# Kernel tuning notes

Hardware: AMD Instinct MI355X
Metric: run time of the kernel (lower is better)

## Reference

```python
import jax, jax.numpy as jnp
import numpy as np

EPS = 0.5
MIN_SAMPLES = 5


def setup_inputs() -> dict:
    key = jax.random.key(0)
    X = jax.random.uniform(key, (12288, 8), dtype=jnp.float32)
    return {"X": X}


def reference(X):
    """DBSCAN: eps-range queries + cluster expansion, expressed as
    eps-graph connected components over core points (same clustering
    as the serial BFS in the original module; cluster ids are assigned
    in order of each cluster's minimum core index, matching the
    ascending-scan discovery order of the original)."""
    N = X.shape[0]
    SENTINEL = jnp.int32(N)

    # pairwise squared Euclidean distances [N, N] (KDTree range query equivalent)
    sq = jnp.sum(X * X, axis=1)
    d2 = sq[:, None] + sq[None, :] - 2.0 * (X @ X.T)
    adj = d2 <= (EPS * EPS)                      # eps-neighborhood (includes self)

    density = jnp.sum(adj, axis=1)               # |query_ball_point(x_i, eps)|
    core = density >= MIN_SAMPLES                # core-point mask

    # core-core edges: BFS expansion only propagates through cores
    core_adj = adj & core[None, :] & core[:, None]

    idx = jnp.arange(N, dtype=jnp.int32)
    init = jnp.where(core, idx, SENTINEL)        # each core starts as its own root

    def prop(lbl):
        # min label over core neighbors (min-plus propagation = connected components)
        nb_min = jnp.min(jnp.where(core_adj, lbl[None, :], SENTINEL), axis=1)
        return jnp.minimum(lbl, nb_min)

    def cond(state):
        cur, prev = state
        return jnp.any(cur != prev)

    def body(state):
        cur, _ = state
        return prop(cur), cur

    lbl, _ = jax.lax.while_loop(cond, body, (prop(init), init))

    # border points: non-core points within eps of a core join that core's cluster
    core_nb = jnp.min(jnp.where(adj & core[None, :], lbl[None, :], SENTINEL), axis=1)
    root = jnp.where(core, lbl, core_nb)         # SENTINEL -> noise

    # compact cluster ids: rank of each cluster root (min core index) ascending,
    # matching the original's sequential discovery order k = 0, 1, ...
    is_root = core & (lbl == idx)
    rank = jnp.cumsum(is_root.astype(jnp.int32)) - 1   # rank[i] valid where is_root[i]
    labels = jnp.where(root < SENTINEL,
                       rank[jnp.clip(root, 0, N - 1)],
                       jnp.int32(-1))
    return labels
```

## Files before the change

kernel.cpp:

```cpp
#include <hip/hip_runtime.h>

#define NPTS 12288
#define DIMS 8
#define EPS2 0.25f
#define MINS 5
#define NIB1 (NPTS / 256)
#define NW   (NPTS / 32)
#define SENT NPTS
#define RMAX 512
#define W    (RMAX / 32)
#define BIGL 0x3fffffff
#define FT   128
#define FB   256
#define FBGRID 256

#define ATHR 128
#define AROWS 4
#define ATI  (ATHR * AROWS)
#define ANIB (NPTS / ATI)
#define ANJB 48
#define AJC  (NPTS / ANJB)
#define AWCH (AJC / 32)

__device__ __forceinline__ float dist2(const float* xi, const float4& a, const float4& b,
                                       float sqi, float sqj) {
  float dot = 0.f;
  dot = fmaf(xi[0], a.x, dot); dot = fmaf(xi[1], a.y, dot);
  dot = fmaf(xi[2], a.z, dot); dot = fmaf(xi[3], a.w, dot);
  dot = fmaf(xi[4], b.x, dot); dot = fmaf(xi[5], b.y, dot);
  dot = fmaf(xi[6], b.z, dot); dot = fmaf(xi[7], b.w, dot);
  return (sqi + sqj) - 2.0f * dot;
}


__global__ __launch_bounds__(ATHR) void k_adj(const float* __restrict__ X,
                                              unsigned int* __restrict__ adj,
                                              int* __restrict__ density) {
  __shared__ float4 xs[AJC][2];
  __shared__ float sqs[AJC];
  int t = threadIdx.x;
  int j0 = blockIdx.y * AJC;
  for (int s = t; s < AJC; s += ATHR) {
    int j = j0 + s;
    float4 a = ((const float4*)X)[j * 2];
    float4 b = ((const float4*)X)[j * 2 + 1];
    xs[s][0] = a; xs[s][1] = b;
    float sv = 0.f;
    sv = fmaf(a.x, a.x, sv); sv = fmaf(a.y, a.y, sv); sv = fmaf(a.z, a.z, sv); sv = fmaf(a.w, a.w, sv);
    sv = fmaf(b.x, b.x, sv); sv = fmaf(b.y, b.y, sv); sv = fmaf(b.z, b.z, sv); sv = fmaf(b.w, b.w, sv);
    sqs[s] = sv;
  }
  int ib = blockIdx.x * ATI + t;
  float xi[AROWS][DIMS];
  float sqi[AROWS];
#pragma unroll
  for (int r = 0; r < AROWS; r++) {
    int i = ib + r * ATHR;
#pragma unroll
    for (int d = 0; d < DIMS; d++) xi[r][d] = X[i * DIMS + d];
    float sv = 0.f;
#pragma unroll
    for (int d = 0; d < DIMS; d++) sv = fmaf(xi[r][d], xi[r][d], sv);
    sqi[r] = sv;
  }
  __syncthreads();
  unsigned int acc[AROWS][AWCH];
#pragma unroll
  for (int w = 0; w < AWCH; w++) {
    unsigned int b0 = 0u, b1 = 0u, b2 = 0u, b3 = 0u;
#pragma unroll 4
    for (int bit = 0; bit < 32; bit++) {
      int jj = (w << 5) + bit;
      float4 xa = xs[jj][0], xb = xs[jj][1];
      float sj = sqs[jj];
      unsigned int m = 1u << bit;
      if (dist2(xi[0], xa, xb, sqi[0], sj) <= EPS2) b0 |= m;
      if (dist2(xi[1], xa, xb, sqi[1], sj) <= EPS2) b1 |= m;
      if (dist2(xi[2], xa, xb, sqi[2], sj) <= EPS2) b2 |= m;
      if (dist2(xi[3], xa, xb, sqi[3], sj) <= EPS2) b3 |= m;
    }
    acc[0][w] = b0; acc[1][w] = b1; acc[2][w] = b2; acc[3][w] = b3;
  }
#pragma unroll
  for (int r = 0; r < AROWS; r++) {
    int i = ib + r * ATHR;
    uint4* dst = (uint4*)(adj + (size_t)i * NW + blockIdx.y * AWCH);
    dst[0] = make_uint4(acc[r][0], acc[r][1], acc[r][2], acc[r][3]);
    dst[1] = make_uint4(acc[r][4], acc[r][5], acc[r][6], acc[r][7]);
    int pc = 0;
#pragma unroll
    for (int w = 0; w < AWCH; w++) pc += __popc(acc[r][w]);
    atomicAdd(&density[i], pc);
  }
}

__global__ __launch_bounds__(256) void k_core(const int* __restrict__ density,
                                              unsigned long long* __restrict__ corebm,
                                              unsigned int* __restrict__ bm) {
  int t = threadIdx.x;
  if (blockIdx.x == 0) {
#pragma unroll
    for (int q = 0; q < RMAX * W / 256; q++) bm[t + q * 256] = 0u;
  }
  int i = blockIdx.x * 256 + t;
  unsigned long long m = __ballot(density[i] >= MINS);
  if ((t & 63) == 0) corebm[i >> 6] = m;
}

__global__ __launch_bounds__(256) void k_hookbm(const unsigned int* __restrict__ adj,
                                                const unsigned int* __restrict__ cb32,
                                                int* __restrict__ hook) {
  __shared__ unsigned int cb[NW];
  int t = threadIdx.x;
  for (int w = t; w < NW; w += 256) cb[w] = cb32[w];
  __syncthreads();
  int i = blockIdx.x * 256 + t;
  const unsigned int* row = adj + (size_t)i * NW;
  int m = i;
  for (int w = 0; w < NW; w++) {
    unsigned int x = row[w] & cb[w];
    if (x) { m = min(m, (w << 5) + __ffs(x) - 1); break; }
  }
  hook[i] = m;
}

__global__ __launch_bounds__(256) void k_compress(const int* __restrict__ density,
                                                  const int* __restrict__ hook,
                                                  int* __restrict__ L0) {
  int i = blockIdx.x * blockDim.x + threadIdx.x;
  if (i >= NPTS) return;
  if (density[i] >= MINS) {
    int v = i;
    int h = hook[v];
    while (h != v) { v = h; h = hook[v]; }
    L0[i] = v;
  } else {
    L0[i] = i;
  }
}

__global__ __launch_bounds__(1024) void k_rid(const int* __restrict__ density,
                                              const int* __restrict__ L0,
                                              int* __restrict__ Rptr,
                                              int* __restrict__ labL,
                                              int* __restrict__ bcount) {
  __shared__ unsigned short ridS[NPTS];
  __shared__ int wsum[16];
  int t = threadIdx.x;
  int lane = t & 63, wid = t >> 6;
  const int SEG = NPTS / 1024;
  int base = t * SEG;
  int flags = 0;
  int s = 0;
#pragma unroll
  for (int k = 0; k < SEG; k++) {
    int i = base + k;
    int f = (density[i] >= MINS && L0[i] == i) ? 1 : 0;
    flags |= f << k;
    s += f;
  }
  int segsum = s;
#pragma unroll
  for (int off = 1; off < 64; off <<= 1) {
    int n = __shfl_up(s, off, 64);
    if (lane >= off) s += n;
  }
  if (lane == 63) wsum[wid] = s;
  __syncthreads();
  int woff = 0;
  for (int w = 0; w < wid; w++) woff += wsum[w];
  int run = woff + s - segsum;
#pragma unroll
  for (int k = 0; k < SEG; k++) {
    ridS[base + k] = (unsigned short)run;
    run += (flags >> k) & 1;
  }
  if (t == 1023) *Rptr = run;
  if (t == 0) *bcount = 0;
  __syncthreads();
#pragma unroll
  for (int k = 0; k < SEG; k++) {
    int i = base + k;
    labL[i] = (density[i] >= MINS) ? min((int)ridS[L0[i]], RMAX - 1) : -1;
  }
}

__global__ __launch_bounds__(FB) void k_fillbm(const unsigned int* __restrict__ adj,
                                               const unsigned int* __restrict__ cb32,
                                               const int* __restrict__ labL,
                                               unsigned int* __restrict__ bm) {
  __shared__ unsigned int bmL[RMAX * W];
  __shared__ unsigned short labS[NPTS];
  __shared__ unsigned int cb[NW];
  int t = threadIdx.x;
  for (int q = t; q < RMAX * W; q += FB) bmL[q] = 0u;
  for (int q = t; q < NPTS; q += FB) labS[q] = (unsigned short)(labL[q] + 1);
  for (int w = t; w < NW; w += FB) cb[w] = cb32[w];
  __syncthreads();
  int lane = t & 63, wv = t >> 6;
  int gw = blockIdx.x * 4 + wv;
  for (int i = gw; i < NPTS; i += 4 * FBGRID) {
    int a0 = (int)labS[i] - 1;
    if (a0 < 0) continue;
    const unsigned int* row = adj + (size_t)i * NW;
    int wi = i >> 5;
    for (int w = wi + lane; w < NW; w += 64) {
      unsigned int x = row[w] & cb[w];
      if (w == wi) x &= (0xFFFFFFFEu << (i & 31));
      while (x) {
        int b = __ffs(x) - 1; x &= x - 1;
        int lj = (int)labS[(w << 5) + b] - 1;
        if (lj != a0) {
          atomicOr(&bmL[a0 * W + (lj >> 5)], 1u << (lj & 31));
          atomicOr(&bmL[lj * W + (a0 >> 5)], 1u << (a0 & 31));
        }
      }
    }
  }
  __syncthreads();
  for (int q = t; q < RMAX * W; q += FB) {
    unsigned int v = bmL[q];
    if (v) atomicOr(&bm[q], v);
  }
}

__global__ __launch_bounds__(RMAX) void k_cc(const unsigned int* __restrict__ bm,
                                             const int* __restrict__ Rptr,
                                             int* __restrict__ clab) {
  __shared__ int lbl[RMAX];
  __shared__ int mn[RMAX];
  __shared__ int chg, cmp;
  int a = threadIdx.x;
  int R = *Rptr; if (R > RMAX) R = RMAX;
  lbl[a] = a;
  __syncthreads();
  while (true) {
    int m = lbl[a];
    if (a < R) {
      const unsigned int* row = bm + a * W;
#pragma unroll
      for (int w = 0; w < W; w++) {
        unsigned int bits = row[w];
        while (bits) {
          int b = __ffs(bits) - 1;
          bits &= bits - 1;
          m = min(m, lbl[(w << 5) + b]);
        }
      }
    }
    mn[a] = m;
    if (a == 0) chg = 0;
    __syncthreads();
    int l = lbl[a];
    if (m < l) { atomicMin(&lbl[l], m); atomicMin(&lbl[a], m); chg = 1; }
    __syncthreads();
    while (true) {
      if (a == 0) cmp = 0;
      __syncthreads();
      int nl = lbl[lbl[a]];
      __syncthreads();
      if (nl < lbl[a]) { lbl[a] = nl; cmp = 1; }
      __syncthreads();
      if (!cmp) break;
    }
    if (!chg) break;
    __syncthreads();
  }
  int flag = (a < R && lbl[a] == a) ? 1 : 0;
  mn[a] = flag;
  __syncthreads();
  for (int off = 1; off < RMAX; off <<= 1) {
    int v = mn[a];
    int add = (a >= off) ? mn[a - off] : 0;
    __syncthreads();
    mn[a] = v + add;
    __syncthreads();
  }
  clab[a] = mn[lbl[a]] - 1;
}

__global__ __launch_bounds__(256) void k_labels(const int* __restrict__ labL,
                                                const int* __restrict__ clab,
                                                int* __restrict__ labArr,
                                                int* __restrict__ blist,
                                                int* __restrict__ bcount,
                                                float* __restrict__ out) {
  int i = blockIdx.x * blockDim.x + threadIdx.x;
  if (i >= NPTS) return;
  int a = labL[i];
  if (a >= 0) {
    int lab = clab[a];
    labArr[i] = lab;
    out[i] = (float)lab;
  } else {
    labArr[i] = BIGL;
    out[i] = -1.0f;
    int pos = atomicAdd(bcount, 1);
    blist[pos] = i;
  }
}

__global__ __launch_bounds__(FT) void k_border(const unsigned int* __restrict__ adj,
                                               const unsigned int* __restrict__ cb32,
                                               const int* __restrict__ labArr,
                                               const int* __restrict__ blist,
                                               const int* __restrict__ bcount,
                                               float* __restrict__ out) {
  __shared__ unsigned int cb[NW];
  __shared__ int wm[FT / 64];
  int t = threadIdx.x;
  for (int w = t; w < NW; w += FT) cb[w] = cb32[w];
  __syncthreads();
  int count = *bcount;
  for (int k = blockIdx.x; k < count; k += gridDim.x) {
    int p = blist[k];
    const unsigned int* row = adj + (size_t)p * NW;
    int m = BIGL;
    for (int w = t; w < NW; w += FT) {
      unsigned int x = row[w] & cb[w];
      while (x) {
        int b = __ffs(x) - 1; x &= x - 1;
        m = min(m, labArr[(w << 5) + b]);
      }
    }
#pragma unroll
    for (int off = 32; off >= 1; off >>= 1) m = min(m, __shfl_xor(m, off, 64));
    if ((t & 63) == 0) wm[t >> 6] = m;
    __syncthreads();
    if (t == 0) {
      int mm = min(wm[0], wm[1]);
      out[p] = (mm < BIGL) ? (float)mm : -1.0f;
    }
    __syncthreads();
  }
}


extern "C" void kernel_launch(void* const* d_in, const int* in_sizes, int n_in,
                              void* d_out, int out_size, void* d_ws, size_t ws_size,
                              hipStream_t stream) {
  const float* X = (const float*)d_in[0];
  float* out = (float*)d_out;

  char* ws = (char*)d_ws;
  unsigned int* adj = (unsigned int*)ws;
  size_t off = (size_t)NPTS * NW * 4;
  int* density = (int*)(ws + off);           off += 4 * NPTS;
  int* hook    = (int*)(ws + off);           off += 4 * NPTS;
  int* L0      = (int*)(ws + off);           off += 4 * NPTS;
  int* labL    = (int*)(ws + off);           off += 4 * NPTS;
  int* blist   = (int*)(ws + off);           off += 4 * NPTS;
  unsigned long long* corebm = (unsigned long long*)(ws + off); off += 2048;
  unsigned int* bm  = (unsigned int*)(ws + off); off += 4 * RMAX * W;
  int* clab    = (int*)(ws + off);           off += 4 * RMAX;
  int* Rptr    = (int*)(ws + off);
  int* bcount  = Rptr + 1;
  int* labArr  = L0;

  hipMemsetAsync(density, 0, 4 * NPTS, stream);

  dim3 gridA(ANIB, ANJB);

  k_adj<<<gridA, ATHR, 0, stream>>>(X, adj, density);
  k_core<<<NIB1, 256, 0, stream>>>(density, corebm, bm);
  k_hookbm<<<NIB1, 256, 0, stream>>>(adj, (const unsigned int*)corebm, hook);
  k_compress<<<NIB1, 256, 0, stream>>>(density, hook, L0);
  k_rid<<<1, 1024, 0, stream>>>(density, L0, Rptr, labL, bcount);
  k_fillbm<<<FBGRID, FB, 0, stream>>>(adj, (const unsigned int*)corebm, labL, bm);
  k_cc<<<1, RMAX, 0, stream>>>(bm, Rptr, clab);
  k_labels<<<NIB1, 256, 0, stream>>>(labL, clab, labArr, blist, bcount, out);
  k_border<<<256, FT, 0, stream>>>(adj, (const unsigned int*)corebm, labArr, blist, bcount, out);
}
```

Measured before the change: 240.3 us.

## Use packed FMA in adjacency kernel, bound hook scan, fuse compress into rid

The adjacency kernel now uses 256 threads with 2 rows each and computes dot products with two-wide float vector FMAs, which can map to packed fp32 instructions. The hook kernel scans only the words up to the point's own index, since only lower-index core neighbours can lower the hook. The separate pointer-chasing compress kernel is removed and its root-finding loop moved into the single-block rid kernel, saving one launch but running serial chains inside one block. labArr gets its own buffer now that L0 is gone.

```diff
diff --git a/kernel.cpp b/kernel.cpp
--- a/kernel.cpp
+++ b/kernel.cpp
@@ -14,22 +14,23 @@
 #define FB   256
 #define FBGRID 256
 
-#define ATHR 128
-#define AROWS 4
+#define ATHR 256
+#define AROWS 2
 #define ATI  (ATHR * AROWS)
 #define ANIB (NPTS / ATI)
 #define ANJB 48
 #define AJC  (NPTS / ANJB)
 #define AWCH (AJC / 32)
 
-__device__ __forceinline__ float dist2(const float* xi, const float4& a, const float4& b,
-                                       float sqi, float sqj) {
-  float dot = 0.f;
-  dot = fmaf(xi[0], a.x, dot); dot = fmaf(xi[1], a.y, dot);
-  dot = fmaf(xi[2], a.z, dot); dot = fmaf(xi[3], a.w, dot);
-  dot = fmaf(xi[4], b.x, dot); dot = fmaf(xi[5], b.y, dot);
-  dot = fmaf(xi[6], b.z, dot); dot = fmaf(xi[7], b.w, dot);
-  return (sqi + sqj) - 2.0f * dot;
+typedef float v2f __attribute__((ext_vector_type(2)));
+
+__device__ __forceinline__ float dot8(const v2f* xi, const float4& a, const float4& b) {
+  v2f y0 = {a.x, a.y}, y1 = {a.z, a.w}, y2 = {b.x, b.y}, y3 = {b.z, b.w};
+  v2f d = xi[0] * y0;
+  d = __builtin_elementwise_fma(xi[1], y1, d);
+  d = __builtin_elementwise_fma(xi[2], y2, d);
+  d = __builtin_elementwise_fma(xi[3], y3, d);
+  return d.x + d.y;
 }
 
 
@@ -40,58 +41,61 @@
   __shared__ float sqs[AJC];
   int t = threadIdx.x;
   int j0 = blockIdx.y * AJC;
-  for (int s = t; s < AJC; s += ATHR) {
-    int j = j0 + s;
+  {
+    int j = j0 + t;
     float4 a = ((const float4*)X)[j * 2];
     float4 b = ((const float4*)X)[j * 2 + 1];
-    xs[s][0] = a; xs[s][1] = b;
+    xs[t][0] = a; xs[t][1] = b;
     float sv = 0.f;
     sv = fmaf(a.x, a.x, sv); sv = fmaf(a.y, a.y, sv); sv = fmaf(a.z, a.z, sv); sv = fmaf(a.w, a.w, sv);
     sv = fmaf(b.x, b.x, sv); sv = fmaf(b.y, b.y, sv); sv = fmaf(b.z, b.z, sv); sv = fmaf(b.w, b.w, sv);
-    sqs[s] = sv;
-  }
-  int ib = blockIdx.x * ATI + t;
-  float xi[AROWS][DIMS];
-  float sqi[AROWS];
-#pragma unroll
-  for (int r = 0; r < AROWS; r++) {
-    int i = ib + r * ATHR;
-#pragma unroll
-    for (int d = 0; d < DIMS; d++) xi[r][d] = X[i * DIMS + d];
-    float sv = 0.f;
-#pragma unroll
-    for (int d = 0; d < DIMS; d++) sv = fmaf(xi[r][d], xi[r][d], sv);
-    sqi[r] = sv;
-  }
-  __syncthreads();
-  unsigned int acc[AROWS][AWCH];
+    sqs[t] = sv;
+  }
+  int i0 = blockIdx.x * ATI + t, i1 = i0 + ATHR;
+  v2f xi0[4], xi1[4];
+  {
+    float4 a0 = ((const float4*)X)[i0 * 2], b0v = ((const float4*)X)[i0 * 2 + 1];
+    float4 a1 = ((const float4*)X)[i1 * 2], b1v = ((const float4*)X)[i1 * 2 + 1];
+    xi0[0] = (v2f){a0.x, a0.y}; xi0[1] = (v2f){a0.z, a0.w};
+    xi0[2] = (v2f){b0v.x, b0v.y}; xi0[3] = (v2f){b0v.z, b0v.w};
+    xi1[0] = (v2f){a1.x, a1.y}; xi1[1] = (v2f){a1.z, a1.w};
+    xi1[2] = (v2f){b1v.x, b1v.y}; xi1[3] = (v2f){b1v.z, b1v.w};
+  }
+  float sq0 = 0.f, sq1 = 0.f;
+#pragma unroll
+  for (int q = 0; q < 4; q++) {
+    v2f p0 = xi0[q] * xi0[q], p1 = xi1[q] * xi1[q];
+    sq0 += p0.x + p0.y; sq1 += p1.x + p1.y;
+  }
+  __syncthreads();
+  unsigned int acc0[AWCH], acc1[AWCH];
 #pragma unroll
   for (int w = 0; w < AWCH; w++) {
-    unsigned int b0 = 0u, b1 = 0u, b2 = 0u, b3 = 0u;
+    unsigned int b0 = 0u, b1 = 0u;
 #pragma unroll 4
     for (int bit = 0; bit < 32; bit++) {
       int jj = (w << 5) + bit;
       float4 xa = xs[jj][0], xb = xs[jj][1];
       float sj = sqs[jj];
       unsigned int m = 1u << bit;
-      if (dist2(xi[0], xa, xb, sqi[0], sj) <= EPS2) b0 |= m;
-      if (dist2(xi[1], xa, xb, sqi[1], sj) <= EPS2) b1 |= m;
-      if (dist2(xi[2], xa, xb, sqi[2], sj) <= EPS2) b2 |= m;
-      if (dist2(xi[3], xa, xb, sqi[3], sj) <= EPS2) b3 |= m;
-    }
-    acc[0][w] = b0; acc[1][w] = b1; acc[2][w] = b2; acc[3][w] = b3;
-  }
-#pragma unroll
-  for (int r = 0; r < AROWS; r++) {
-    int i = ib + r * ATHR;
-    uint4* dst = (uint4*)(adj + (size_t)i * NW + blockIdx.y * AWCH);
-    dst[0] = make_uint4(acc[r][0], acc[r][1], acc[r][2], acc[r][3]);
-    dst[1] = make_uint4(acc[r][4], acc[r][5], acc[r][6], acc[r][7]);
-    int pc = 0;
-#pragma unroll
-    for (int w = 0; w < AWCH; w++) pc += __popc(acc[r][w]);
-    atomicAdd(&density[i], pc);
-  }
+      float d20 = (sq0 + sj) - 2.0f * dot8(xi0, xa, xb);
+      float d21 = (sq1 + sj) - 2.0f * dot8(xi1, xa, xb);
+      if (d20 <= EPS2) b0 |= m;
+      if (d21 <= EPS2) b1 |= m;
+    }
+    acc0[w] = b0; acc1[w] = b1;
+  }
+  uint4* dst0 = (uint4*)(adj + (size_t)i0 * NW + blockIdx.y * AWCH);
+  uint4* dst1 = (uint4*)(adj + (size_t)i1 * NW + blockIdx.y * AWCH);
+  dst0[0] = make_uint4(acc0[0], acc0[1], acc0[2], acc0[3]);
+  dst0[1] = make_uint4(acc0[4], acc0[5], acc0[6], acc0[7]);
+  dst1[0] = make_uint4(acc1[0], acc1[1], acc1[2], acc1[3]);
+  dst1[1] = make_uint4(acc1[4], acc1[5], acc1[6], acc1[7]);
+  int pc0 = 0, pc1 = 0;
+#pragma unroll
+  for (int w = 0; w < AWCH; w++) { pc0 += __popc(acc0[w]); pc1 += __popc(acc1[w]); }
+  atomicAdd(&density[i0], pc0);
+  atomicAdd(&density[i1], pc1);
 }
 
 __global__ __launch_bounds__(256) void k_core(const int* __restrict__ density,
@@ -116,31 +120,18 @@
   __syncthreads();
   int i = blockIdx.x * 256 + t;
   const unsigned int* row = adj + (size_t)i * NW;
+  int wi = i >> 5;
   int m = i;
-  for (int w = 0; w < NW; w++) {
+  for (int w = 0; w <= wi; w++) {
     unsigned int x = row[w] & cb[w];
-    if (x) { m = min(m, (w << 5) + __ffs(x) - 1); break; }
+    if (w == wi) x &= (1u << (i & 31)) - 1;
+    if (x) { m = (w << 5) + __ffs(x) - 1; break; }
   }
   hook[i] = m;
 }
 
-__global__ __launch_bounds__(256) void k_compress(const int* __restrict__ density,
-                                                  const int* __restrict__ hook,
-                                                  int* __restrict__ L0) {
-  int i = blockIdx.x * blockDim.x + threadIdx.x;
-  if (i >= NPTS) return;
-  if (density[i] >= MINS) {
-    int v = i;
-    int h = hook[v];
-    while (h != v) { v = h; h = hook[v]; }
-    L0[i] = v;
-  } else {
-    L0[i] = i;
-  }
-}
-
 __global__ __launch_bounds__(1024) void k_rid(const int* __restrict__ density,
-                                              const int* __restrict__ L0,
+                                              const int* __restrict__ hook,
                                               int* __restrict__ Rptr,
                                               int* __restrict__ labL,
                                               int* __restrict__ bcount) {
@@ -155,7 +146,7 @@
 #pragma unroll
   for (int k = 0; k < SEG; k++) {
     int i = base + k;
-    int f = (density[i] >= MINS && L0[i] == i) ? 1 : 0;
+    int f = (density[i] >= MINS && hook[i] == i) ? 1 : 0;
     flags |= f << k;
     s += f;
   }
@@ -178,10 +169,15 @@
   if (t == 1023) *Rptr = run;
   if (t == 0) *bcount = 0;
   __syncthreads();
-#pragma unroll
   for (int k = 0; k < SEG; k++) {
     int i = base + k;
-    labL[i] = (density[i] >= MINS) ? min((int)ridS[L0[i]], RMAX - 1) : -1;
+    int lab = -1;
+    if (density[i] >= MINS) {
+      int v = i, h = hook[v];
+      while (h != v) { v = h; h = hook[v]; }
+      lab = min((int)ridS[v], RMAX - 1);
+    }
+    labL[i] = lab;
   }
 }
 
@@ -347,15 +343,14 @@
   size_t off = (size_t)NPTS * NW * 4;
   int* density = (int*)(ws + off);           off += 4 * NPTS;
   int* hook    = (int*)(ws + off);           off += 4 * NPTS;
-  int* L0      = (int*)(ws + off);           off += 4 * NPTS;
   int* labL    = (int*)(ws + off);           off += 4 * NPTS;
+  int* labArr  = (int*)(ws + off);           off += 4 * NPTS;
   int* blist   = (int*)(ws + off);           off += 4 * NPTS;
   unsigned long long* corebm = (unsigned long long*)(ws + off); off += 2048;
   unsigned int* bm  = (unsigned int*)(ws + off); off += 4 * RMAX * W;
   int* clab    = (int*)(ws + off);           off += 4 * RMAX;
   int* Rptr    = (int*)(ws + off);
   int* bcount  = Rptr + 1;
-  int* labArr  = L0;
 
   hipMemsetAsync(density, 0, 4 * NPTS, stream);
 
@@ -364,8 +359,7 @@
   k_adj<<<gridA, ATHR, 0, stream>>>(X, adj, density);
   k_core<<<NIB1, 256, 0, stream>>>(density, corebm, bm);
   k_hookbm<<<NIB1, 256, 0, stream>>>(adj, (const unsigned int*)corebm, hook);
-  k_compress<<<NIB1, 256, 0, stream>>>(density, hook, L0);
-  k_rid<<<1, 1024, 0, stream>>>(density, L0, Rptr, labL, bcount);
+  k_rid<<<1, 1024, 0, stream>>>(density, hook, Rptr, labL, bcount);
   k_fillbm<<<FBGRID, FB, 0, stream>>>(adj, (const unsigned int*)corebm, labL, bm);
   k_cc<<<1, RMAX, 0, stream>>>(bm, Rptr, clab);
   k_labels<<<NIB1, 256, 0, stream>>>(labL, clab, labArr, blist, bcount, out);
```

New measurement: 228.2 us. 5.0% less time.
